# Kernel optimization log

Measured on AMD Instinct MI355X. Metric: run time of the kernel, lower is better.

## Reference

```python
import math
import jax, jax.numpy as jnp
import numpy as np

NUM_HEADS = 32

def _alibi_slopes(n: int) -> jnp.ndarray:
    cp2 = 2 ** int(math.floor(math.log2(n)))
    base = 2.0 ** (-(2.0 ** (-(math.log2(cp2) - 3))))
    slopes = base ** np.arange(1, cp2 + 1, dtype=np.float64)
    if cp2 != n:
        extra_base = 2.0 ** (-(2.0 ** (-(math.log2(2 * cp2) - 3))))
        rem = min(cp2, n - cp2)
        slopes = np.concatenate([slopes, extra_base ** np.arange(1, 1 + 2 * rem, 2, dtype=np.float64)])
    return jnp.asarray(slopes, dtype=jnp.float32)


def setup_inputs() -> dict:
    key = jax.random.key(0)
    k1, k2, k3 = jax.random.split(key, 3)
    B, S, E, H, D = 2, 2048, 4096, NUM_HEADS, 128
    hidden_states = jax.random.normal(k1, (B, S, E), dtype=jnp.float32)
    # torch Linear y = x @ W^T; we store transposed weights [in, out]
    w_qkv = jax.random.normal(k2, (E, H * D + 2 * D), dtype=jnp.float32) * 0.02
    w_c = jax.random.normal(k3, (E, E), dtype=jnp.float32) * 0.02
    return {"hidden_states": hidden_states, "w_qkv": w_qkv, "w_c": w_c}


def reference(hidden_states, w_qkv, w_c):
    B, S, E = hidden_states.shape
    H = NUM_HEADS
    D = E // H
    scaling = D ** -0.5

    qkv = hidden_states @ w_qkv                      # [B,S,H*D+2D]
    q = qkv[..., : H * D].reshape(B, S, H, D)        # [B,S,H,D]
    k = qkv[..., H * D: H * D + D]                   # [B,S,D] single KV head (MQA)
    v = qkv[..., H * D + D:]                         # [B,S,D]

    pos = jnp.arange(S)
    slopes = _alibi_slopes(H)                        # [H]
    # ALiBi: slope * (k_pos - q_pos), <= 0 in the causal region
    bias = slopes[:, None, None] * (pos[None, None, :] - pos[None, :, None]).astype(jnp.float32)  # [H,S,S]

    scores = jnp.einsum('bqhd,bkd->bhqk', q, k) * scaling + bias[None]  # [B,H,S,S]
    causal = pos[:, None] >= pos[None, :]            # [S,S]
    scores = jnp.where(causal[None, None], scores, jnp.finfo(scores.dtype).min)
    probs = jax.nn.softmax(scores, axis=-1)
    attn = jnp.einsum('bhqk,bkd->bqhd', probs, v).reshape(B, S, E)
    return attn @ w_c
```

## Files before the change

### kernel.cpp

```cpp
#include <hip/hip_runtime.h>
#include <hip/hip_bf16.h>

typedef unsigned short u16;
typedef unsigned int u32;
typedef __attribute__((ext_vector_type(8))) short s16x8;
typedef __attribute__((ext_vector_type(4))) float f32x4;

#define MFMA_BF16(a, b, c) __builtin_amdgcn_mfma_f32_16x16x32_bf16(a, b, c, 0, 0, 0)

__device__ __forceinline__ u16 f2bf(float f) {
  union { float f; u32 u; } c; c.f = f;
  return (u16)((c.u + 0x7FFFu + ((c.u >> 16) & 1u)) >> 16);
}

__device__ __forceinline__ u32 pkbf(float a, float b) {
  float2 t; t.x = a; t.y = b;
  __hip_bfloat162 h = __float22bfloat162_rn(t);
  union { __hip_bfloat162 h; u32 u; } c; c.h = h; return c.u;
}

__device__ __forceinline__ void gll16(const void* g, void* l) {
  __builtin_amdgcn_global_load_lds((const __attribute__((address_space(1))) void*)g,
                                   (__attribute__((address_space(3))) void*)l, 16, 0, 0);
}

__device__ __forceinline__ f32x4 f4zero() { f32x4 z = {0.f, 0.f, 0.f, 0.f}; return z; }

__global__ void cvt_bf16_kernel(const float4* __restrict__ in, u16* __restrict__ out, int n4) {
  int i = blockIdx.x * 256 + threadIdx.x;
  if (i >= n4) return;
  float4 v = in[i];
  uint2 w;
  w.x = (u32)f2bf(v.x) | ((u32)f2bf(v.y) << 16);
  w.y = (u32)f2bf(v.z) | ((u32)f2bf(v.w) << 16);
  *reinterpret_cast<uint2*>(out + (size_t)i * 4) = w;
}

__global__ void transpose_cvt_frag_kernel(const float* __restrict__ in, u16* __restrict__ out,
                                          int R, int C) {
  __shared__ float tile[32][33];
  int tx = threadIdx.x, ty = threadIdx.y;
  int r0 = blockIdx.y * 32, c0 = blockIdx.x * 32;
#pragma unroll
  for (int i = 0; i < 32; i += 8)
    tile[ty + i][tx] = in[(size_t)(r0 + ty + i) * C + c0 + tx];
  __syncthreads();
  const int KT = R >> 5;
  const int kt = r0 >> 5;
  const int q = tx >> 3, e = tx & 7;
#pragma unroll
  for (int i = 0; i < 32; i += 8) {
    const int n = c0 + ty + i;
    const int nb = n >> 4, li2 = n & 15;
    out[((size_t)nb * KT + kt) * 512 + (q * 16 + li2) * 8 + e] = f2bf(tile[tx][ty + i]);
  }
}


#define BARRIER __builtin_amdgcn_s_barrier()
#define SCHEDB __builtin_amdgcn_sched_barrier(0)
#define PRIO1 __builtin_amdgcn_s_setprio(1)
#define PRIO0 __builtin_amdgcn_s_setprio(0)
#define VM1 asm volatile("s_waitcnt vmcnt(1)" ::: "memory")
#define VM0 asm volatile("s_waitcnt vmcnt(0)" ::: "memory")
#define NOPW do {} while (0)

#define PAB(P) ((P) * 8192)

#define RDA(P) do { _Pragma("unroll")                                                    \
  for (int mi2 = 0; mi2 < 4; ++mi2)                                                      \
    a[mi2] = *(const s16x8*)(smem + PAB(P) + aOff + mi2*1024);                           \
} while (0)

#define LDB(T) do { _Pragma("unroll")                                                    \
  for (int ni2 = 0; ni2 < 4; ++ni2)                                                      \
    b[ni2] = *(const s16x8*)(Bw + ((size_t)ni2 * 128 + (T)) * 512);                      \
} while (0)

#define MFMA16 do { _Pragma("unroll")                                                    \
  for (int mi2 = 0; mi2 < 4; ++mi2) { _Pragma("unroll")                                  \
    for (int ni2 = 0; ni2 < 4; ++ni2)                                                    \
      acc[mi2][ni2] = MFMA_BF16(a[mi2], b[ni2], acc[mi2][ni2]);                          \
  } } while (0)

#define STAGE1(P, kn) gll16(srcA + (kn), smem + PAB(P) + tt*16)

#define TILE_S(PR, PS, T) do {                                                           \
  s16x8 a[4], b[4];                                                                      \
  LDB(T);                                                                                \
  RDA(PR);                                                                               \
  STAGE1(PS, ((T) + 2) * 32);                                                            \
  SCHEDB;                                                                                \
  PRIO1; MFMA16; PRIO0;                                                                  \
  SCHEDB;                                                                                \
  VM1;                                                                                   \
  BARRIER;                                                                               \
} while (0)

#define TILE_T(PR, T, WAIT) do {                                                         \
  s16x8 a[4], b[4];                                                                      \
  LDB(T);                                                                                \
  RDA(PR);                                                                               \
  SCHEDB;                                                                                \
  PRIO1; MFMA16; PRIO0;                                                                  \
  SCHEDB;                                                                                \
  WAIT;                                                                                  \
  BARRIER;                                                                               \
} while (0)

template<int EPI>
__global__ __launch_bounds__(512, 4)
void gemm128_kernel(const u16* __restrict__ A, const u16* __restrict__ Bf,
                    float* __restrict__ Cf, u16* __restrict__ Cq,
                    u16* __restrict__ Ck, u16* __restrict__ Cvt,
                    int N) {
  __shared__ __align__(16) char smem[24576];
  const int tt = threadIdx.x;
  const int w = tt >> 6, l = tt & 63;
  const int li = l & 15, g = l >> 4;
  const int wm = w >> 2, wn = w & 3;

  const int gx = gridDim.x;
  const int nwg = gx * gridDim.y;
  int id = blockIdx.y * gx + blockIdx.x;
  id = (id & 7) * (nwg >> 3) + (id >> 3);
  const int bn = id % gx, bm = id / gx;

  f32x4 acc[4][4];
#pragma unroll
  for (int i = 0; i < 4; ++i)
#pragma unroll
    for (int j = 0; j < 4; ++j) acc[i][j] = f4zero();

  const int sg = (tt & 7) ^ ((tt >> 3) & 7);
  const int ar = 2 * (tt >> 3) + (sg >> 2);
  const int aq = sg & 3;
  const u16* srcA = A + (size_t)(bm * 128 + ar) * 4096 + aq * 8;

  const u16* Bw = Bf + ((size_t)(bn * 16 + wn * 4) * 128) * 512 + l * 8;

  const int slot = (((li & 1) * 4 + g) ^ ((li >> 1) & 7)) * 16;
  const int aOff = wm * 4096 + (li >> 1) * 128 + slot;

  STAGE1(0, 0);
  STAGE1(1, 32);
  VM1;
  BARRIER;

  for (int t3 = 0; t3 < 126; t3 += 3) {
    TILE_S(0, 2, t3);
    TILE_S(1, 0, t3 + 1);
    TILE_S(2, 1, t3 + 2);
  }
  TILE_T(0, 126, VM0);
  TILE_T(1, 127, NOPW);

#pragma unroll
  for (int mi = 0; mi < 4; ++mi) {
#pragma unroll
    for (int ni = 0; ni < 4; ++ni) {
      const int row0 = bm * 128 + wm * 64 + mi * 16 + g * 4;
      const int col = bn * 256 + wn * 64 + ni * 16 + li;
#pragma unroll
      for (int r = 0; r < 4; ++r) {
        const int m = row0 + r;
        const float v = acc[mi][ni][r];
        if (EPI == 0) {
          Cf[(size_t)m * N + col] = v;
        } else {
          const int bb2 = m >> 11, s = m & 2047;
          const int kt = s >> 5;
          const size_t tb = (size_t)(bb2 * 64 + kt);
          if (col < 4096) {
            Cq[(size_t)m * 4096 + col] = f2bf(v);
          } else if (col < 4224) {
            const int d = col - 4096, kr = s & 31;
            const int mk = kr >> 4, lii = kr & 15;
            const int kk = d >> 5, gg = (d >> 3) & 3, e = d & 7;
            Ck[(tb * 8 + mk * 4 + kk) * 512 + (gg * 16 + lii) * 8 + e] = f2bf(v);
          } else {
            const int d = col - 4224, kp = s & 31;
            const int mf = d >> 4, lii = d & 15;
            const int gg = kp >> 3, e = kp & 7;
            Cvt[(tb * 8 + mf) * 512 + (gg * 16 + lii) * 8 + e] = f2bf(v);
          }
        }
      }
    }
  }
}


__device__ __forceinline__ void load_ktile(s16x8 (&dst)[8], const u16* kf, size_t tb, int l) {
#pragma unroll
  for (int f = 0; f < 8; ++f)
    dst[f] = *(const s16x8*)&kf[(tb * 8 + f) * 512 + l * 8];
}

template<bool DIAG>
__device__ __forceinline__ void attn_tile(
    int kt, const u16* kf, const u16* vf, size_t bb64, int l, int li, int g,
    s16x8 (&use)[8], s16x8 (&fill)[8], bool do_fill,
    const s16x8 (&bq)[2][4], f32x4 (&acc)[8][2],
    float (&m_)[2], float (&lp)[2], float (&bias)[2],
    float c1, const float (&cjr)[8], float bstep, u16 (*Pw)[40]) {
  const size_t tb = bb64 + kt;
  s16x8 vr[8];
#pragma unroll
  for (int f = 0; f < 8; ++f)
    vr[f] = *(const s16x8*)&vf[(tb * 8 + f) * 512 + l * 8];
  if (do_fill) load_ktile(fill, kf, tb - 1, l);

  f32x4 sc[2][2];
  sc[0][0] = f4zero(); sc[0][1] = f4zero(); sc[1][0] = f4zero(); sc[1][1] = f4zero();
#pragma unroll
  for (int kk = 0; kk < 4; ++kk)
#pragma unroll
    for (int mk = 0; mk < 2; ++mk) {
      sc[mk][0] = MFMA_BF16(use[mk * 4 + kk], bq[0][kk], sc[mk][0]);
      sc[mk][1] = MFMA_BF16(use[mk * 4 + kk], bq[1][kk], sc[mk][1]);
    }

#pragma unroll
  for (int nq = 0; nq < 2; ++nq) {
    float sv[8];
    float pm = -3e38f;
    if (DIAG) {
#pragma unroll
      for (int mk = 0; mk < 2; ++mk)
#pragma unroll
        for (int r = 0; r < 4; ++r) {
          const int kd = mk * 16 + g * 4 + r - (nq * 16 + li);
          float s = fmaf(sc[mk][nq][r], c1, bias[nq] + cjr[mk * 4 + r]);
          s = (kd <= 0) ? s : -1e30f;
          sv[mk * 4 + r] = s;
          pm = fmaxf(pm, s);
        }
      pm = fmaxf(pm, __shfl_xor(pm, 16));
      pm = fmaxf(pm, __shfl_xor(pm, 32));
      m_[nq] = pm;
    } else {
#pragma unroll
      for (int mk = 0; mk < 2; ++mk)
#pragma unroll
        for (int r = 0; r < 4; ++r) {
          float s = fmaf(sc[mk][nq][r], c1, bias[nq] + cjr[mk * 4 + r]);
          sv[mk * 4 + r] = s;
          pm = fmaxf(pm, s);
        }
      if (__any(pm > m_[nq])) {
        pm = fmaxf(pm, __shfl_xor(pm, 16));
        pm = fmaxf(pm, __shfl_xor(pm, 32));
        const float nm = fmaxf(m_[nq], pm);
        const float scale = exp2f(m_[nq] - nm);
#pragma unroll
        for (int mf = 0; mf < 8; ++mf) acc[mf][nq] *= scale;
        lp[nq] *= scale;
        m_[nq] = nm;
      }
    }
    const float mref = m_[nq];
    float e[8];
#pragma unroll
    for (int j = 0; j < 8; ++j) e[j] = exp2f(sv[j] - mref);
    lp[nq] += ((e[0] + e[1]) + (e[2] + e[3])) + ((e[4] + e[5]) + (e[6] + e[7]));
#pragma unroll
    for (int mk = 0; mk < 2; ++mk) {
      uint2 wv;
      wv.x = pkbf(e[mk * 4 + 0], e[mk * 4 + 1]);
      wv.y = pkbf(e[mk * 4 + 2], e[mk * 4 + 3]);
      *reinterpret_cast<uint2*>(&Pw[nq * 16 + li][mk * 16 + g * 4]) = wv;
    }
    bias[nq] -= bstep;
  }

  s16x8 pb0 = *(const s16x8*)&Pw[li][g * 8];
  s16x8 pb1 = *(const s16x8*)&Pw[16 + li][g * 8];
#pragma unroll
  for (int mf = 0; mf < 8; ++mf) {
    acc[mf][0] = MFMA_BF16(vr[mf], pb0, acc[mf][0]);
    acc[mf][1] = MFMA_BF16(vr[mf], pb1, acc[mf][1]);
  }
}

__device__ __forceinline__ void attn_qtile(
    int qt, int h, int b, const u16* qbuf, const u16* kf, const u16* vf,
    u16* obuf, int l, int li, int g, float c1, float sl2, u16 (*Pw)[40]) {
  const int S = 2048;
  const int q0 = qt * 32;
  const size_t bb64 = (size_t)b * 64;

  s16x8 bq[2][4];
#pragma unroll
  for (int nq = 0; nq < 2; ++nq)
#pragma unroll
    for (int kk = 0; kk < 4; ++kk)
      bq[nq][kk] = *(const s16x8*)&qbuf[(size_t)(b * S + q0 + nq * 16 + li) * 4096
                                        + h * 128 + kk * 32 + g * 8];

  f32x4 acc[8][2];
#pragma unroll
  for (int mf = 0; mf < 8; ++mf) { acc[mf][0] = f4zero(); acc[mf][1] = f4zero(); }
  float m_[2] = {-3e38f, -3e38f};
  float lp[2] = {0.f, 0.f};

  float cjr[8];
#pragma unroll
  for (int j = 0; j < 8; ++j) cjr[j] = sl2 * (float)((j >> 2) * 16 + (j & 3));
  float bias[2];
#pragma unroll
  for (int nq = 0; nq < 2; ++nq)
    bias[nq] = sl2 * (float)(g * 4 - nq * 16 - li);
  const float bstep = sl2 * 32.f;

  s16x8 kA[8], kB[8];
  load_ktile(kA, kf, bb64 + qt, l);
  attn_tile<true>(qt, kf, vf, bb64, l, li, g, kA, kB, qt >= 1,
                  bq, acc, m_, lp, bias, c1, cjr, bstep, Pw);
  int kt = qt - 1;
  while (kt >= 1) {
    attn_tile<false>(kt, kf, vf, bb64, l, li, g, kB, kA, true,
                     bq, acc, m_, lp, bias, c1, cjr, bstep, Pw);
    attn_tile<false>(kt - 1, kf, vf, bb64, l, li, g, kA, kB, kt >= 2,
                     bq, acc, m_, lp, bias, c1, cjr, bstep, Pw);
    kt -= 2;
  }
  if (kt == 0)
    attn_tile<false>(0, kf, vf, bb64, l, li, g, kB, kA, false,
                     bq, acc, m_, lp, bias, c1, cjr, bstep, Pw);

#pragma unroll
  for (int nq = 0; nq < 2; ++nq) {
    float ls = lp[nq];
    ls += __shfl_xor(ls, 16);
    ls += __shfl_xor(ls, 32);
    const float inv = 1.f / ls;
    const size_t rowbase = (size_t)(b * S + q0 + nq * 16 + li) * 4096 + h * 128;
#pragma unroll
    for (int mf = 0; mf < 8; ++mf) {
      f32x4 v = acc[mf][nq];
      uint2 wv;
      wv.x = pkbf(v[0] * inv, v[1] * inv);
      wv.y = pkbf(v[2] * inv, v[3] * inv);
      *reinterpret_cast<uint2*>(&obuf[rowbase + mf * 16 + g * 4]) = wv;
    }
  }
}

__global__ __launch_bounds__(64, 2)
void attn_kernel(const u16* __restrict__ qbuf, const u16* __restrict__ kf,
                 const u16* __restrict__ vf, u16* __restrict__ obuf) {
  const int p = blockIdx.x, h = blockIdx.y, b = blockIdx.z;
  const int l = threadIdx.x, li = l & 15, g = l >> 4;
  const float L2E = 1.4426950408889634f;
  const float slope = exp2f(-0.25f * (float)(h + 1));
  const float c1 = 0.08838834764831845f * L2E;
  const float sl2 = slope * L2E;
  __shared__ __align__(16) u16 P[32][40];
  attn_qtile(63 - p, h, b, qbuf, kf, vf, obuf, l, li, g, c1, sl2, P);
  attn_qtile(p, h, b, qbuf, kf, vf, obuf, l, li, g, c1, sl2, P);
}

extern "C" void kernel_launch(void* const* d_in, const int* in_sizes, int n_in,
                              void* d_out, int out_size, void* d_ws, size_t ws_size,
                              hipStream_t stream) {
  (void)in_sizes; (void)n_in; (void)out_size; (void)ws_size;
  const float* hidden = (const float*)d_in[0];
  const float* w_qkv = (const float*)d_in[1];
  const float* w_c = (const float*)d_in[2];
  float* out = (float*)d_out;
  char* ws = (char*)d_ws;

  u16* hid_bf = (u16*)(ws + 0);
  u16* wT     = (u16*)(ws + 33554432);
  u16* qbuf   = (u16*)(ws + 69206016);
  u16* kbuf   = (u16*)(ws + 102760448);
  u16* vtbuf  = (u16*)(ws + 103809024);

  cvt_bf16_kernel<<<16384, 256, 0, stream>>>((const float4*)hidden, hid_bf, 4194304);
  transpose_cvt_frag_kernel<<<dim3(136, 128), dim3(32, 8), 0, stream>>>(w_qkv, wT, 4096, 4352);
  gemm128_kernel<1><<<dim3(17, 32), 512, 0, stream>>>(hid_bf, wT, nullptr, qbuf, kbuf, vtbuf,
                                                      4352);
  attn_kernel<<<dim3(32, 32, 2), 64, 0, stream>>>(qbuf, kbuf, vtbuf, hid_bf);
  transpose_cvt_frag_kernel<<<dim3(128, 128), dim3(32, 8), 0, stream>>>(w_c, wT, 4096, 4096);
  gemm128_kernel<0><<<dim3(16, 32), 512, 0, stream>>>(hid_bf, wT, out, nullptr, nullptr, nullptr,
                                                      4096);
}
```

Before: 502.6 us.

## Prefetch B fragments one tile ahead with double-buffered registers and remap block ids

B operand fragments are now loaded directly from global memory one k-tile ahead into alternating register sets, so their latency is hidden behind the current tile's MFMAs. Before, each tile loaded B and consumed it in the same step. Wait counts are changed to allow the extra outstanding loads. The workgroup-to-tile mapping is also replaced with a fixed bit-sliced scheme that assumes a specific grid shape. In exchange, register pressure goes up, and the new mapping is only correct for that grid size.

```diff
diff --git a/kernel.cpp b/kernel.cpp
--- a/kernel.cpp
+++ b/kernel.cpp
@@ -61,9 +61,9 @@
 #define SCHEDB __builtin_amdgcn_sched_barrier(0)
 #define PRIO1 __builtin_amdgcn_s_setprio(1)
 #define PRIO0 __builtin_amdgcn_s_setprio(0)
+#define VM5 asm volatile("s_waitcnt vmcnt(5)" ::: "memory")
+#define VM4 asm volatile("s_waitcnt vmcnt(4)" ::: "memory")
 #define VM1 asm volatile("s_waitcnt vmcnt(1)" ::: "memory")
-#define VM0 asm volatile("s_waitcnt vmcnt(0)" ::: "memory")
-#define NOPW do {} while (0)
 
 #define PAB(P) ((P) * 8192)
 
@@ -72,39 +72,28 @@
     a[mi2] = *(const s16x8*)(smem + PAB(P) + aOff + mi2*1024);                           \
 } while (0)
 
-#define LDB(T) do { _Pragma("unroll")                                                    \
+#define LDB(BSET, T) do { _Pragma("unroll")                                              \
   for (int ni2 = 0; ni2 < 4; ++ni2)                                                      \
-    b[ni2] = *(const s16x8*)(Bw + ((size_t)ni2 * 128 + (T)) * 512);                      \
+    BSET[ni2] = *(const s16x8*)(Bw + ((size_t)ni2 * 128 + (T)) * 512);                   \
 } while (0)
 
-#define MFMA16 do { _Pragma("unroll")                                                    \
+#define MFMA16(BSET) do { _Pragma("unroll")                                              \
   for (int mi2 = 0; mi2 < 4; ++mi2) { _Pragma("unroll")                                  \
     for (int ni2 = 0; ni2 < 4; ++ni2)                                                    \
-      acc[mi2][ni2] = MFMA_BF16(a[mi2], b[ni2], acc[mi2][ni2]);                          \
+      acc[mi2][ni2] = MFMA_BF16(a[mi2], BSET[ni2], acc[mi2][ni2]);                       \
   } } while (0)
 
 #define STAGE1(P, kn) gll16(srcA + (kn), smem + PAB(P) + tt*16)
 
-#define TILE_S(PR, PS, T) do {                                                           \
-  s16x8 a[4], b[4];                                                                      \
-  LDB(T);                                                                                \
-  RDA(PR);                                                                               \
+#define TILE(PR, PS, T, BU, BL) do {                                                     \
+  s16x8 a[4];                                                                            \
+  LDB(BL, (T) + 1);                                                                      \
   STAGE1(PS, ((T) + 2) * 32);                                                            \
-  SCHEDB;                                                                                \
-  PRIO1; MFMA16; PRIO0;                                                                  \
-  SCHEDB;                                                                                \
-  VM1;                                                                                   \
-  BARRIER;                                                                               \
-} while (0)
-
-#define TILE_T(PR, T, WAIT) do {                                                         \
-  s16x8 a[4], b[4];                                                                      \
-  LDB(T);                                                                                \
   RDA(PR);                                                                               \
   SCHEDB;                                                                                \
-  PRIO1; MFMA16; PRIO0;                                                                  \
+  PRIO1; MFMA16(BU); PRIO0;                                                              \
   SCHEDB;                                                                                \
-  WAIT;                                                                                  \
+  VM5;                                                                                   \
   BARRIER;                                                                               \
 } while (0)
 
@@ -121,10 +110,9 @@
   const int wm = w >> 2, wn = w & 3;
 
   const int gx = gridDim.x;
-  const int nwg = gx * gridDim.y;
-  int id = blockIdx.y * gx + blockIdx.x;
-  id = (id & 7) * (nwg >> 3) + (id >> 3);
-  const int bn = id % gx, bm = id / gx;
+  const int raw = blockIdx.y * gx + blockIdx.x;
+  const int bn = raw >> 5;
+  const int bm = ((raw >> 3) & 3) * 8 + (raw & 7);
 
   f32x4 acc[4][4];
 #pragma unroll
@@ -142,18 +130,38 @@
   const int slot = (((li & 1) * 4 + g) ^ ((li >> 1) & 7)) * 16;
   const int aOff = wm * 4096 + (li >> 1) * 128 + slot;
 
+  s16x8 bA[4], bB[4];
+
+  LDB(bA, 0);
   STAGE1(0, 0);
   STAGE1(1, 32);
   VM1;
   BARRIER;
 
-  for (int t3 = 0; t3 < 126; t3 += 3) {
-    TILE_S(0, 2, t3);
-    TILE_S(1, 0, t3 + 1);
-    TILE_S(2, 1, t3 + 2);
-  }
-  TILE_T(0, 126, VM0);
-  TILE_T(1, 127, NOPW);
+  for (int t6 = 0; t6 < 126; t6 += 6) {
+    TILE(0, 2, t6 + 0, bA, bB);
+    TILE(1, 0, t6 + 1, bB, bA);
+    TILE(2, 1, t6 + 2, bA, bB);
+    TILE(0, 2, t6 + 3, bB, bA);
+    TILE(1, 0, t6 + 4, bA, bB);
+    TILE(2, 1, t6 + 5, bB, bA);
+  }
+  {
+    s16x8 a[4];
+    LDB(bB, 127);
+    RDA(0);
+    SCHEDB;
+    PRIO1; MFMA16(bA); PRIO0;
+    SCHEDB;
+    VM4;
+    BARRIER;
+  }
+  {
+    s16x8 a[4];
+    RDA(1);
+    SCHEDB;
+    PRIO1; MFMA16(bB); PRIO0;
+  }
 
 #pragma unroll
   for (int mi = 0; mi < 4; ++mi) {
```

Result: slower. 644.7 us (+28.3%).
